# Performance work log

Hardware: AMD Instinct MI355X
Metric: run time of the kernel (lower is better)

Reference implementation:

```python
import jax, jax.numpy as jnp
import numpy as np

B, L, D = 512, 200, 128
N_ITEMS = 50001
T_STEPS = 4
TAU = 2.0
STEP = 1
V_TH = 1.0
SG_ALPHA = 4.0  # spikingjelly default surrogate.Sigmoid alpha


@jax.custom_vjp
def spike(x):
    return (x >= 0.0).astype(x.dtype)

def _spike_fwd(x):
    return spike(x), x

def _spike_bwd(x, g):
    s = jax.nn.sigmoid(SG_ALPHA * x)
    return (g * SG_ALPHA * s * (1.0 - s),)

spike.defvjp(_spike_fwd, _spike_bwd)


def lif_multistep(x):
    """Multi-step LIF (hard reset to 0, detach_reset). x: [T, ...] -> spikes [T, ...]."""
    def step(v, xt):
        v = v + (xt - v) / TAU  # charge (v_reset = 0)
        s = spike(v - V_TH)
        v = v - jax.lax.stop_gradient(s) * v  # hard reset, detached spike
        return v, s
    v0 = jnp.zeros_like(x[0])
    _, spikes = jax.lax.scan(step, v0, x)
    return spikes


def layernorm(x, g, b, eps=1e-5):
    m = x.mean(-1, keepdims=True)
    v = x.var(-1, keepdims=True)
    return (x - m) / jnp.sqrt(v + eps) * g + b


def _build_session_graphs(rng):
    lens = rng.integers(50, L + 1, size=B)
    item_seq = np.zeros((B, L), dtype=np.int64)
    for b in range(B):
        item_seq[b, :lens[b]] = rng.integers(1, N_ITEMS, size=lens[b])
    alias = np.zeros((B, L), dtype=np.int64)
    items = np.zeros((B, L), dtype=np.int64)
    A = np.zeros((B, L, 2 * L), dtype=np.float32)
    for b in range(B):
        u = item_seq[b]
        node = np.unique(u)  # sorted
        items[b, :len(node)] = node
        alias[b] = np.searchsorted(node, u)
        uA = np.zeros((L, L), dtype=np.float32)
        for i in range(L - 1):
            if u[i + 1] == 0:
                break
            r = np.searchsorted(node, u[i])
            c = np.searchsorted(node, u[i + 1])
            uA[r, c] = 1.0
        sin = uA.sum(0); sin[sin == 0] = 1.0
        sout = uA.sum(1); sout[sout == 0] = 1.0
        A[b, :, :L] = (uA / sin).T          # u_A_in.T
        A[b, :, L:] = ((uA.T / sout)).T     # u_A_out.T
    mask = item_seq > 0
    return A, alias, items, mask, lens.astype(np.int64)


def setup_inputs() -> dict:
    rng = np.random.default_rng(0)
    A, alias, items, mask, lens = _build_session_graphs(rng)
    stdv = 1.0 / np.sqrt(D)
    key = jax.random.key(0)
    ks = jax.random.split(key, 24)
    u = lambda k, shape: jax.random.uniform(k, shape, jnp.float32, -stdv, stdv)
    item_emb = u(ks[0], (N_ITEMS, D)).at[0].set(0.0)  # padding_idx=0
    return {
        "A": jnp.asarray(A),
        "alias_inputs": jnp.asarray(alias),
        "items": jnp.asarray(items),
        "mask": jnp.asarray(mask),
        "item_seq_len": jnp.asarray(lens),
        "item_emb": item_emb,
        "W_in": u(ks[1], (D, D)), "b_in": u(ks[2], (D,)),
        "W_out": u(ks[3], (D, D)), "b_out": u(ks[4], (D,)),
        "w_ih": u(ks[5], (3 * D, 2 * D)), "w_hh": u(ks[6], (3 * D, D)),
        "b_ih": u(ks[7], (3 * D,)), "b_hh": u(ks[8], (3 * D,)),
        "b_iah": u(ks[9], (D,)), "b_ioh": u(ks[10], (D,)),
        "W1": u(ks[11], (D, D)), "W2": u(ks[12], (D, D)),
        "W3": u(ks[13], (1, D)), "Wt": u(ks[14], (D, 2 * D)),
        "g_q": u(ks[15], (D,)), "beta_q": u(ks[16], (D,)),
        "g_sh": u(ks[17], (2 * D,)), "beta_sh": u(ks[18], (2 * D,)),
    }


def _forward(A, alias_inputs, items, mask, item_seq_len, item_emb,
             W_in, b_in, W_out, b_out, w_ih, w_hh, b_ih, b_hh, b_iah, b_ioh,
             W1, W2, W3, Wt, g_q, beta_q, g_sh, beta_sh):
    hidden = item_emb[items]  # [B,L,D]
    for _ in range(STEP):
        ein = hidden @ W_in.T + b_in
        eout = hidden @ W_out.T + b_out
        input_in = jnp.einsum('bij,bjd->bid', A[:, :, :L], ein) + b_iah
        input_out = jnp.einsum('bij,bjd->bid', A[:, :, L:], eout) + b_ioh
        inputs = jnp.concatenate([input_in, input_out], axis=-1)  # [B,L,2D]
        gi = inputs @ w_ih.T + b_ih  # [B,L,3D]
        gh = hidden @ w_hh.T + b_hh
        i_r, i_i, i_n = jnp.split(gi, 3, axis=-1)
        h_r, h_i, h_n = jnp.split(gh, 3, axis=-1)
        r = jax.nn.sigmoid(i_r + h_r)
        z = jax.nn.sigmoid(i_i + h_i)
        n = jnp.tanh(i_n + r * h_n)
        hidden = (1.0 - z) * hidden + z * n
    seq_hidden = jnp.take_along_axis(hidden, alias_inputs[..., None], axis=1)  # [B,L,D]
    ht = jnp.take_along_axis(seq_hidden, (item_seq_len - 1)[:, None, None], axis=1)[:, 0]  # [B,D]
    Qb = (ht @ W1.T)[:, None, :] + seq_hidden @ W2.T  # [B,L,D]
    Q = jnp.broadcast_to(Qb[None], (T_STEPS, B, L, D))
    Qs = lif_multistep(layernorm(Q, g_q, beta_q))
    alpha = Qs @ W3.T  # [T,B,L,1]
    mf = mask.astype(alpha.dtype)
    a = jnp.sum(alpha * seq_hidden[None] * mf[None, :, :, None], axis=2)  # [T,B,D]
    ht_T = jnp.broadcast_to(ht[None], (T_STEPS, B, D))
    sh = jnp.concatenate([a, ht_T], axis=-1)  # [T,B,2D]
    sh = layernorm(lif_multistep(sh), g_sh, beta_sh)
    return (sh @ Wt.T).mean(0)  # [B,D]


def reference(A, alias_inputs, items, mask, item_seq_len, item_emb,
              W_in, b_in, W_out, b_out, w_ih, w_hh, b_ih, b_hh, b_iah, b_ioh,
              W1, W2, W3, Wt, g_q, beta_q, g_sh, beta_sh):
    return _forward(A, alias_inputs, items, mask, item_seq_len, item_emb,
                    W_in, b_in, W_out, b_out, w_ih, w_hh, b_ih, b_hh, b_iah, b_ioh,
                    W1, W2, W3, Wt, g_q, beta_q, g_sh, beta_sh)
```

## Files before the change

kernel.cpp:

```cpp
#include <hip/hip_runtime.h>
#include <hip/hip_bf16.h>
#include <cstdint>
#include <cstddef>

#define B_ 512
#define L_ 200
#define D_ 128
#define M_ (B_*L_)
#define T_ 4

typedef short bf16x8 __attribute__((ext_vector_type(8)));
typedef unsigned short u16x8 __attribute__((ext_vector_type(8)));
typedef float f32x4 __attribute__((ext_vector_type(4)));

__device__ __forceinline__ float bf2f(unsigned short u){
  union { unsigned int i; float f; } c; c.i = ((unsigned int)u)<<16; return c.f;
}
__device__ __forceinline__ unsigned short f2bf(float f){
  union { float f; unsigned int i; } c; c.f = f;
  unsigned int r = c.i + 0x7FFFu + ((c.i>>16)&1u);
  return (unsigned short)(r>>16);
}
__device__ __forceinline__ float wsum(float v){
  #pragma unroll
  for (int m=1;m<64;m<<=1) v += __shfl_xor(v, m, 64);
  return v;
}
__device__ __forceinline__ void gload_lds16(const void* g, void* l){
  __builtin_amdgcn_global_load_lds(
      (const __attribute__((address_space(1))) void*)g,
      (__attribute__((address_space(3))) void*)l, 16, 0, 0);
}

__global__ __launch_bounds__(128)
void k_prepW(const float* __restrict__ w_ih, const float* __restrict__ w_hh,
             const float* __restrict__ W_in, const float* __restrict__ W_out,
             const float* __restrict__ b_in, const float* __restrict__ b_out,
             const float* __restrict__ b_ih, const float* __restrict__ b_hh,
             const float* __restrict__ b_iah, const float* __restrict__ b_ioh,
             const float* __restrict__ W2,
             const int* __restrict__ alias, const int* __restrict__ lens,
             unsigned short* __restrict__ Wbig, float* __restrict__ biasBase,
             float* __restrict__ uIn, float* __restrict__ uOut,
             unsigned short* __restrict__ w2b, int* __restrict__ nb)
{
  const int p = blockIdx.x, t = threadIdx.x;
  if (p < 128) w2b[p*128 + t] = f2bf(W2[p*128 + t]);
  const int dim = p>>2, g = p&3;
  const int row = (g==0) ? dim : (g==1) ? 128+dim : 256+dim;
  const bool has_ih = (g!=3), has_hh = (g!=2);
  __shared__ float wl[128], wrg[128], red[3][128];
  wl[t]  = has_ih ? w_ih[(size_t)row*256 + t]       : 0.f;
  wrg[t] = has_ih ? w_ih[(size_t)row*256 + 128 + t] : 0.f;
  __syncthreads();
  float cin = 0.f, cout = 0.f;
  if (has_ih) {
    for (int m=0;m<128;m++){
      cin  += wl[m]  * W_in [m*128 + t];
      cout += wrg[m] * W_out[m*128 + t];
    }
  }
  Wbig[(size_t)p*384 +       t] = f2bf(cin);
  Wbig[(size_t)p*384 + 128 + t] = f2bf(cout);
  Wbig[(size_t)p*384 + 256 + t] = f2bf(has_hh ? w_hh[(size_t)row*128 + t] : 0.f);
  red[0][t] = wl[t]*b_iah[t] + wrg[t]*b_ioh[t];
  red[1][t] = wl[t]*b_in[t];
  red[2][t] = wrg[t]*b_out[t];
  __syncthreads();
  if (t == 0) {
    float v=0.f, ui=0.f, uo=0.f;
    for (int k=0;k<128;k++){ v += red[0][k]; ui += red[1][k]; uo += red[2][k]; }
    float bb;
    if (g==0)      bb = b_ih[dim]     + b_hh[dim]     + v;
    else if (g==1) bb = b_ih[128+dim] + b_hh[128+dim] + v;
    else if (g==2) bb = b_ih[256+dim] + v;
    else           bb = b_hh[256+dim];
    biasBase[p] = bb;
    uIn[p]  = has_ih ? ui : 0.f;
    uOut[p] = has_ih ? uo : 0.f;
  }
  if (t < 64) {
    const int len = lens[p];
    int m = 0;
    for (int l=t; l<len; l+=64) m = max(m, alias[p*L_ + l]);
    #pragma unroll
    for (int o=1;o<64;o<<=1) m = max(m, __shfl_xor(m, o, 64));
    if (t==0) nb[p] = m + 1;
  }
}

__global__ __launch_bounds__(512)
void k_scan(const int* __restrict__ nb, const int* __restrict__ lens,
            int* __restrict__ nbase, int* __restrict__ vbase)
{
  __shared__ int A[2][512], Bv[2][512];
  const int t = threadIdx.x;
  const int a0 = nb[t], b0 = lens[t];
  A[0][t] = a0; Bv[0][t] = b0;
  __syncthreads();
  int cur = 0;
  for (int off=1; off<512; off<<=1){
    const int nxt = cur^1;
    A[nxt][t]  = A[cur][t]  + (t>=off ? A[cur][t-off]  : 0);
    Bv[nxt][t] = Bv[cur][t] + (t>=off ? Bv[cur][t-off] : 0);
    __syncthreads();
    cur = nxt;
  }
  nbase[t] = A[cur][t] - a0;
  vbase[t] = Bv[cur][t] - b0;
  if (t==511){ nbase[512] = A[cur][511]; vbase[512] = Bv[cur][511]; }
}

__global__ __launch_bounds__(1024)
void k_aggemb(const int* __restrict__ alias, const int* __restrict__ items,
              const int* __restrict__ lens, const float* __restrict__ emb,
              const int* __restrict__ nb, const int* __restrict__ nbase,
              const int* __restrict__ vbase,
              unsigned short* __restrict__ X3, unsigned char* __restrict__ cf,
              int* __restrict__ gidx)
{
  const int b = blockIdx.x, tid = threadIdx.x;
  __shared__ unsigned short hl[L_*128];
  __shared__ int al[L_], it[L_];
  __shared__ unsigned bmIn[L_*8], bmOut[L_*8];
  if (tid < L_) { al[tid] = alias[b*L_ + tid]; it[tid] = items[b*L_ + tid]; }
  for (int i=tid; i<L_*8; i+=1024){ bmIn[i]=0u; bmOut[i]=0u; }
  __syncthreads();
  const int len = lens[b], nB = nb[b], base = nbase[b];
  if (tid < len) gidx[vbase[b] + tid] = base + al[tid];
  if (tid < len-1) {
    const int r = al[tid], c = al[tid+1];
    atomicOr(&bmIn[c*8 + (r>>5)],  1u<<(r&31));
    atomicOr(&bmOut[r*8 + (c>>5)], 1u<<(c&31));
  }
  const int rr = tid>>5, cc = (tid&31)<<2;
  for (int s=0; s<nB; s+=32) {
    const int j = s + rr;
    if (j < nB) {
      const float4 v = *(const float4*)(emb + (size_t)it[j]*128 + cc);
      ushort4 o; o.x=f2bf(v.x); o.y=f2bf(v.y); o.z=f2bf(v.z); o.w=f2bf(v.w);
      *(ushort4*)(hl + j*128 + cc) = o;
      *(ushort4*)(X3 + (size_t)(base + j)*384 + 256 + cc) = o;
    }
  }
  __syncthreads();
  const int g = tid >> 7, d = tid & 127;
  for (int s=0; s<nB; s+=8) {
    const int i = s + g;
    if (i < nB) {
      float si=0.f, so=0.f; int ci=0, co=0;
      #pragma unroll
      for (int wd=0; wd<8; ++wd) {
        unsigned word = bmIn[i*8+wd];
        while (word) { int j = __ffs(word)-1; word &= word-1u;
          si += bf2f(hl[(wd*32+j)*128 + d]); ci++; }
        word = bmOut[i*8+wd];
        while (word) { int j = __ffs(word)-1; word &= word-1u;
          so += bf2f(hl[(wd*32+j)*128 + d]); co++; }
      }
      unsigned short* xr = X3 + (size_t)(base + i)*384;
      xr[d]       = f2bf(si / (float)(ci>0?ci:1));
      xr[128 + d] = f2bf(so / (float)(co>0?co:1));
      if (d == 0) cf[base + i] = (unsigned char)((ci>0?1:0) | (co>0?2:0));
    }
  }
}

__global__ __launch_bounds__(512)
void k_gates_q0(const unsigned short* __restrict__ X3,
                const unsigned short* __restrict__ Wbig,
                const unsigned short* __restrict__ w2b,
                const float* __restrict__ biasBase,
                const float* __restrict__ uIn,
                const float* __restrict__ uOut,
                const unsigned char* __restrict__ cf,
                unsigned short* __restrict__ hidden,
                unsigned short* __restrict__ q0n,
                const int* __restrict__ mlimit)
{
  const int m0 = blockIdx.x * 128;
  if (m0 >= *mlimit) return;
  __shared__ __align__(16) short sA[2][128*32];
  __shared__ __align__(16) short sB[2][512*32];
  const int tid = threadIdx.x;
  const int lane = tid & 63;
  const int w = tid >> 6;
  const int wr  = (w>>2)*64;
  const int wcp = (w&3)*128;
  const int fr = lane & 15;
  const int fq = lane >> 4;
  const int fk = ((fq ^ ((fr>>1)&3))&3)<<3;

  f32x4 acc[4][8];
  #pragma unroll
  for (int i=0;i<4;i++)
    #pragma unroll
    for (int j=0;j<8;j++) acc[i][j] = (f32x4){0.f,0.f,0.f,0.f};

  const int rA = tid>>2, sAx = tid&3;
  const int kA = ((sAx ^ ((rA>>1)&3))&3)<<3;

  auto stage = [&](int t){
    const int buf = t & 1, ks = t << 5;
    gload_lds16(X3 + (size_t)(m0 + rA)*384 + ks + kA, sA[buf] + (size_t)tid*8);
    #pragma unroll
    for (int q=0;q<4;q++){
      const int cB = tid + q*512;
      const int rB = cB>>2, sBx = cB&3;
      const int kB = ((sBx ^ ((rB>>1)&3))&3)<<3;
      gload_lds16(Wbig + (size_t)rB*384 + ks + kB, sB[buf] + (size_t)cB*8);
    }
  };
  stage(0);
  __syncthreads();
  for (int t=0; t<12; ++t){
    if (t < 11) stage(t+1);
    const short* a_ = sA[t&1];
    const short* b_ = sB[t&1];
    bf16x8 af[4], bfr[8];
    #pragma unroll
    for (int i=0;i<4;i++)
      af[i]  = *(const bf16x8*)(a_ + (wr  + i*16 + fr)*32 + fk);
    #pragma unroll
    for (int j=0;j<8;j++)
      bfr[j] = *(const bf16x8*)(b_ + (wcp + j*16 + fr)*32 + fk);
    #pragma unroll
    for (int i=0;i<4;i++)
      #pragma unroll
      for (int j=0;j<8;j++)
        acc[i][j] = __builtin_amdgcn_mfma_f32_16x16x32_bf16(af[i], bfr[j], acc[i][j], 0,0,0);
    __syncthreads();
  }

  short* hl  = sB[0];
  short* w2l = sB[1];

  #pragma unroll
  for (int q=0;q<4;q++){
    const int cW = tid + q*512;
    const int rW = cW>>4, sW = cW&15;
    gload_lds16(w2b + (size_t)rW*128 + ((sW ^ (rW&7))<<3), w2l + (size_t)cW*8);
  }

  const bool q0b = (lane & 1), q1b = (lane & 2);
  #pragma unroll
  for (int j=0;j<8;j++){
    const int dim = (w&3)*32 + j*4 + ((lane>>2)&3);
    const float4 bb = *(const float4*)(biasBase + dim*4);
    const float4 bi = *(const float4*)(uIn  + dim*4);
    const float4 bo = *(const float4*)(uOut + dim*4);
    #pragma unroll
    for (int i=0;i<4;i++){
      const float a0=acc[i][j][0], a1=acc[i][j][1], a2=acc[i][j][2], a3=acc[i][j][3];
      const float t0=__shfl_xor(a0,1), t1=__shfl_xor(a1,1), t2=__shfl_xor(a2,1), t3=__shfl_xor(a3,1);
      const float s0 = q0b? t1:a0, s1 = q0b? a1:t0, s2 = q0b? t3:a2, s3 = q0b? a3:t2;
      const float u0=__shfl_xor(s0,2), u1=__shfl_xor(s1,2), u2=__shfl_xor(s2,2), u3=__shfl_xor(s3,2);
      float G0 = q1b? u2:s0, G1 = q1b? u3:s1, G2 = q1b? s2:u0, G3 = q1b? s3:u1;
      const int row = m0 + wr + i*16 + fq*4 + (lane&3);
      const unsigned c = cf[row];
      const float fi = (c&1) ? 1.f : 0.f, fo = (c&2) ? 1.f : 0.f;
      G0 += bb.x + fi*bi.x + fo*bo.x;
      G1 += bb.y + fi*bi.y + fo*bo.y;
      G2 += bb.z + fi*bi.z + fo*bo.z;
      G3 += bb.w;
      const float h = bf2f(X3[(size_t)row*384 + 256 + dim]);
      const float r = 1.f/(1.f+__expf(-G0));
      const float z = 1.f/(1.f+__expf(-G1));
      const float x = G2 + r*G3;
      const float n = 1.f - 2.f/(__expf(2.f*x)+1.f);
      const unsigned short hv = f2bf((1.f-z)*h + z*n);
      hidden[(size_t)row*128 + dim] = hv;
      const int rl = row - m0;
      hl[rl*128 + (((dim>>3) ^ (rl&7))<<3) + (dim&7)] = hv;
    }
  }
  __syncthreads();

  f32x4 acc2[4][2];
  #pragma unroll
  for (int i=0;i<4;i++){ acc2[i][0]=(f32x4){0,0,0,0}; acc2[i][1]=(f32x4){0,0,0,0}; }
  const int wc2 = (w&3)*32;
  #pragma unroll
  for (int kk=0;kk<4;kk++){
    bf16x8 af2[4], bf2_[2];
    #pragma unroll
    for (int i=0;i<4;i++){
      const int r = wr + i*16 + fr;
      af2[i] = *(const bf16x8*)(hl + r*128 + (((kk*4 + fq) ^ (r&7))<<3));
    }
    #pragma unroll
    for (int j=0;j<2;j++){
      const int c = wc2 + j*16 + fr;
      bf2_[j] = *(const bf16x8*)(w2l + c*128 + (((kk*4 + fq) ^ (c&7))<<3));
    }
    #pragma unroll
    for (int i=0;i<4;i++)
      #pragma unroll
      for (int j=0;j<2;j++)
        acc2[i][j] = __builtin_amdgcn_mfma_f32_16x16x32_bf16(af2[i], bf2_[j], acc2[i][j], 0,0,0);
  }
  #pragma unroll
  for (int i=0;i<4;i++){
    #pragma unroll
    for (int j=0;j<2;j++){
      const int col = wc2 + j*16 + fr;
      #pragma unroll
      for (int v=0;v<4;v++){
        const int row = m0 + wr + i*16 + fq*4 + v;
        q0n[(size_t)row*128 + col] = f2bf(acc2[i][j][v]);
      }
    }
  }
}

__global__ __launch_bounds__(1024)
void k_attn(const unsigned short* __restrict__ q0n,
            const unsigned short* __restrict__ hidden, const int* __restrict__ gidx,
            const int* __restrict__ lens, const int* __restrict__ vbase,
            const float* __restrict__ W1,
            const float* __restrict__ g_q, const float* __restrict__ beta_q,
            const float* __restrict__ W3,
            const float* __restrict__ g_sh, const float* __restrict__ beta_sh,
            const float* __restrict__ Wt, float* __restrict__ out)
{
  const int b = blockIdx.x, tid = threadIdx.x;
  const int w = tid>>6, lane = tid&63;
  __shared__ float a_acc[16][T_][128];
  __shared__ float htv[128], htw[128];
  __shared__ float ys[256];
  __shared__ float part[T_][4];
  const int len = lens[b], vb = vbase[b];
  for (int i=tid; i<16*T_*128; i+=1024) ((float*)a_acc)[i] = 0.f;
  if (tid < 128) htv[tid] = bf2f(hidden[(size_t)gidx[vb + len - 1]*128 + tid]);
  __syncthreads();
  {
    const int d = tid >> 3, seg = (tid & 7) << 4;
    const float* wr1 = W1 + (size_t)d*128 + seg;
    const float* hv = htv + seg;
    float p = 0.f;
    #pragma unroll
    for (int k=0;k<16;k++) p += wr1[k]*hv[k];
    p += __shfl_xor(p, 1, 64); p += __shfl_xor(p, 2, 64); p += __shfl_xor(p, 4, 64);
    if ((tid & 7) == 0) htw[d] = p;
  }
  __syncthreads();
  const float h0 = htw[lane], h1 = htw[lane+64];
  const float gq0 = g_q[lane], gq1 = g_q[lane+64];
  const float bq0 = beta_q[lane], bq1 = beta_q[lane+64];
  const float w30 = W3[lane], w31 = W3[lane+64];
  for (int l = w; l < len; l += 16) {
    const size_t row = (size_t)(vb + l);
    const size_t hrow = (size_t)gidx[row];
    const float q0 = bf2f(q0n[hrow*128 + lane]) + h0;
    const float q1 = bf2f(q0n[hrow*128 + lane + 64]) + h1;
    const float m = wsum(q0+q1) * (1.f/128.f);
    const float d0 = q0-m, d1 = q1-m;
    const float var = wsum(d0*d0 + d1*d1) * (1.f/128.f);
    const float inv = rsqrtf(var + 1e-5f);
    const float x0 = d0*inv*gq0 + bq0;
    const float x1 = d1*inv*gq1 + bq1;
    const float sh0 = bf2f(hidden[hrow*128+lane]), sh1 = bf2f(hidden[hrow*128+lane+64]);
    float v0=0.f, v1=0.f;
    #pragma unroll
    for (int t=0;t<T_;t++){
      v0 = 0.5f*(v0+x0); v1 = 0.5f*(v1+x1);
      const float s0 = (v0>=1.f)?1.f:0.f, s1 = (v1>=1.f)?1.f:0.f;
      v0 -= s0*v0; v1 -= s1*v1;
      const float alpha = wsum(s0*w30 + s1*w31);
      a_acc[w][t][lane] += alpha*sh0; a_acc[w][t][lane+64] += alpha*sh1;
    }
  }
  __syncthreads();

  float sp[T_] = {0.f,0.f,0.f,0.f};
  if (tid < 256) {
    const float xh = (tid >= 128) ? htv[tid-128] : 0.f;
    float v = 0.f;
    #pragma unroll
    for (int t=0;t<T_;t++){
      float x;
      if (tid < 128) {
        x = 0.f;
        #pragma unroll
        for (int p=0;p<16;p++) x += a_acc[p][t][tid];
      } else x = xh;
      v = 0.5f*(v + x);
      const float s = (v>=1.f)?1.f:0.f;
      v -= s*v;
      sp[t] = s;
    }
    #pragma unroll
    for (int t=0;t<T_;t++){
      const float r = wsum(sp[t]);
      if (lane==0) part[t][w] = r;
    }
  }
  __syncthreads();
  if (tid < 256) {
    float acc4 = 0.f;
    #pragma unroll
    for (int t=0;t<T_;t++){
      const float k = part[t][0]+part[t][1]+part[t][2]+part[t][3];
      const float mean = k * (1.f/256.f);
      const float varr = mean - mean*mean;
      const float inv = rsqrtf(varr + 1e-5f);
      acc4 += (sp[t]-mean)*inv;
    }
    ys[tid] = acc4*g_sh[tid] + 4.f*beta_sh[tid];
  }
  __syncthreads();
  if (tid < 128) {
    float acc = 0.f;
    const float4* wr4 = (const float4*)(Wt + (size_t)tid*256);
    const float4* ys4 = (const float4*)ys;
    #pragma unroll 8
    for (int k=0;k<64;k++){
      const float4 wv = wr4[k], yv = ys4[k];
      acc += wv.x*yv.x + wv.y*yv.y + wv.z*yv.z + wv.w*yv.w;
    }
    out[(size_t)b*128 + tid] = acc*0.25f;
  }
}

extern "C" void kernel_launch(void* const* d_in, const int* in_sizes, int n_in,
                              void* d_out, int out_size, void* d_ws, size_t ws_size,
                              hipStream_t stream)
{
  const int*   alias  = (const int*)d_in[1];
  const int*   items  = (const int*)d_in[2];
  const int*   lens   = (const int*)d_in[4];
  const float* emb    = (const float*)d_in[5];
  const float* W_in   = (const float*)d_in[6];
  const float* b_in   = (const float*)d_in[7];
  const float* W_out  = (const float*)d_in[8];
  const float* b_out  = (const float*)d_in[9];
  const float* w_ih   = (const float*)d_in[10];
  const float* w_hh   = (const float*)d_in[11];
  const float* b_ih   = (const float*)d_in[12];
  const float* b_hh   = (const float*)d_in[13];
  const float* b_iah  = (const float*)d_in[14];
  const float* b_ioh  = (const float*)d_in[15];
  const float* W1     = (const float*)d_in[16];
  const float* W2     = (const float*)d_in[17];
  const float* W3     = (const float*)d_in[18];
  const float* Wt     = (const float*)d_in[19];
  const float* g_q    = (const float*)d_in[20];
  const float* beta_q = (const float*)d_in[21];
  const float* g_sh   = (const float*)d_in[22];
  const float* beta_sh= (const float*)d_in[23];

  char* ws = (char*)d_ws;
  size_t off = 0;
  auto alloc = [&](size_t bytes)->void* {
    void* p = ws + off; off += (bytes + 255) & ~(size_t)255; return p;
  };
  unsigned short* X3    = (unsigned short*)alloc((size_t)M_*384*2);
  unsigned short* hidden= (unsigned short*)alloc((size_t)M_*128*2);
  unsigned short* q0n   = (unsigned short*)alloc((size_t)M_*128*2);
  int*            gidx  = (int*)alloc((size_t)M_*4);
  unsigned short* Wbig  = (unsigned short*)alloc((size_t)512*384*2);
  unsigned short* w2b   = (unsigned short*)alloc(16384*2);
  float*          biasBase = (float*)alloc(512*4);
  float*          uIn   = (float*)alloc(512*4);
  float*          uOut  = (float*)alloc(512*4);
  unsigned char*  cf    = (unsigned char*)alloc(M_);
  int*            nb    = (int*)alloc(512*4);
  int*            nbase = (int*)alloc(513*4);
  int*            vbase = (int*)alloc(513*4);
  if (off > ws_size) return;

  k_prepW<<<512,128,0,stream>>>(w_ih,w_hh,W_in,W_out,b_in,b_out,b_ih,b_hh,
                                b_iah,b_ioh,W2,alias,lens,
                                Wbig,biasBase,uIn,uOut,w2b,nb);
  k_scan<<<1,512,0,stream>>>(nb, lens, nbase, vbase);
  k_aggemb<<<B_,1024,0,stream>>>(alias, items, lens, emb, nb, nbase, vbase,
                                 X3, cf, gidx);
  k_gates_q0<<<800,512,0,stream>>>(X3, Wbig, w2b, biasBase, uIn, uOut, cf,
                                   hidden, q0n, nbase+512);
  k_attn<<<B_,1024,0,stream>>>(q0n, hidden, gidx, lens, vbase, W1, g_q, beta_q,
                               W3, g_sh, beta_sh, Wt, (float*)d_out);
}
```

Baseline: 203.2 us.

## Split gates GEMM into two column halves to cut LDS and registers

The fused GRU-gates kernel now computes its 512-wide gate GEMM in two passes of 256 columns. This halves the B-tile shared memory and the accumulator registers per pass, which can raise occupancy. First-half hidden values are packed into registers until the shared buffer is free, and the W2 operand is read straight from global memory into registers instead of being staged in LDS. The cost is reloading and recomputing the A tile (X3) twice, plus extra synchronisation between the passes.

Result: no change. 203.7 us (+0.2%).

```diff
diff --git a/kernel.cpp b/kernel.cpp
--- a/kernel.cpp
+++ b/kernel.cpp
@@ -181,123 +181,133 @@
   const int m0 = blockIdx.x * 128;
   if (m0 >= *mlimit) return;
   __shared__ __align__(16) short sA[2][128*32];
-  __shared__ __align__(16) short sB[2][512*32];
+  __shared__ __align__(16) short sB[2][256*32];
   const int tid = threadIdx.x;
   const int lane = tid & 63;
   const int w = tid >> 6;
   const int wr  = (w>>2)*64;
-  const int wcp = (w&3)*128;
+  const int wcp = (w&3)*64;
   const int fr = lane & 15;
   const int fq = lane >> 4;
   const int fk = ((fq ^ ((fr>>1)&3))&3)<<3;
 
-  f32x4 acc[4][8];
-  #pragma unroll
-  for (int i=0;i<4;i++)
-    #pragma unroll
-    for (int j=0;j<8;j++) acc[i][j] = (f32x4){0.f,0.f,0.f,0.f};
-
-  const int rA = tid>>2, sAx = tid&3;
-  const int kA = ((sAx ^ ((rA>>1)&3))&3)<<3;
-
-  auto stage = [&](int t){
-    const int buf = t & 1, ks = t << 5;
-    gload_lds16(X3 + (size_t)(m0 + rA)*384 + ks + kA, sA[buf] + (size_t)tid*8);
-    #pragma unroll
-    for (int q=0;q<4;q++){
-      const int cB = tid + q*512;
-      const int rB = cB>>2, sBx = cB&3;
-      const int kB = ((sBx ^ ((rB>>1)&3))&3)<<3;
-      gload_lds16(Wbig + (size_t)rB*384 + ks + kB, sB[buf] + (size_t)cB*8);
-    }
-  };
-  stage(0);
-  __syncthreads();
-  for (int t=0; t<12; ++t){
-    if (t < 11) stage(t+1);
-    const short* a_ = sA[t&1];
-    const short* b_ = sB[t&1];
-    bf16x8 af[4], bfr[8];
+  const int ra = tid>>2, sa_ = tid&3, ka = ((sa_ ^ ((ra>>1)&3))&3)<<3;
+  const int c1 = tid + 512, rb1 = c1>>2, sb1 = c1&3, kb1 = ((sb1 ^ ((rb1>>1)&3))&3)<<3;
+
+  short* hl = &sB[0][0];
+  unsigned hv0p[8];
+  const bool q0b_ = (lane & 1), q1b_ = (lane & 2);
+
+  for (int half=0; half<2; ++half){
+    const int p0 = half << 8;
+    f32x4 acc[4][4];
     #pragma unroll
     for (int i=0;i<4;i++)
-      af[i]  = *(const bf16x8*)(a_ + (wr  + i*16 + fr)*32 + fk);
-    #pragma unroll
-    for (int j=0;j<8;j++)
-      bfr[j] = *(const bf16x8*)(b_ + (wcp + j*16 + fr)*32 + fk);
-    #pragma unroll
-    for (int i=0;i<4;i++)
-      #pragma unroll
-      for (int j=0;j<8;j++)
-        acc[i][j] = __builtin_amdgcn_mfma_f32_16x16x32_bf16(af[i], bfr[j], acc[i][j], 0,0,0);
+      #pragma unroll
+      for (int j=0;j<4;j++) acc[i][j] = (f32x4){0.f,0.f,0.f,0.f};
+
+    auto stage = [&](int t){
+      const int buf = t & 1, ks = t << 5;
+      gload_lds16(X3   + (size_t)(m0 + ra )*384 + ks + ka , sA[buf] + (size_t)tid*8);
+      gload_lds16(Wbig + (size_t)(p0 + ra )*384 + ks + ka , sB[buf] + (size_t)tid*8);
+      gload_lds16(Wbig + (size_t)(p0 + rb1)*384 + ks + kb1, sB[buf] + 4096 + (size_t)tid*8);
+    };
+    stage(0);
     __syncthreads();
-  }
-
-  short* hl  = sB[0];
-  short* w2l = sB[1];
-
-  #pragma unroll
-  for (int q=0;q<4;q++){
-    const int cW = tid + q*512;
-    const int rW = cW>>4, sW = cW&15;
-    gload_lds16(w2b + (size_t)rW*128 + ((sW ^ (rW&7))<<3), w2l + (size_t)cW*8);
-  }
-
-  const bool q0b = (lane & 1), q1b = (lane & 2);
-  #pragma unroll
-  for (int j=0;j<8;j++){
-    const int dim = (w&3)*32 + j*4 + ((lane>>2)&3);
-    const float4 bb = *(const float4*)(biasBase + dim*4);
-    const float4 bi = *(const float4*)(uIn  + dim*4);
-    const float4 bo = *(const float4*)(uOut + dim*4);
+    for (int t=0; t<12; ++t){
+      if (t < 11) stage(t+1);
+      const short* a_ = sA[t&1];
+      const short* b_ = sB[t&1];
+      bf16x8 af[4], bfr[4];
+      #pragma unroll
+      for (int i=0;i<4;i++){
+        af[i]  = *(const bf16x8*)(a_ + (wr  + i*16 + fr)*32 + fk);
+        bfr[i] = *(const bf16x8*)(b_ + (wcp + i*16 + fr)*32 + fk);
+      }
+      #pragma unroll
+      for (int i=0;i<4;i++)
+        #pragma unroll
+        for (int j=0;j<4;j++)
+          acc[i][j] = __builtin_amdgcn_mfma_f32_16x16x32_bf16(af[i], bfr[j], acc[i][j], 0,0,0);
+      __syncthreads();
+    }
+
+    #pragma unroll
+    for (int j=0;j<4;j++){
+      const int dim = half*64 + (w&3)*16 + j*4 + ((lane>>2)&3);
+      const float4 bb = *(const float4*)(biasBase + dim*4);
+      const float4 bi = *(const float4*)(uIn  + dim*4);
+      const float4 bo = *(const float4*)(uOut + dim*4);
+      #pragma unroll
+      for (int i=0;i<4;i++){
+        const float a0=acc[i][j][0], a1=acc[i][j][1], a2=acc[i][j][2], a3=acc[i][j][3];
+        const float t0=__shfl_xor(a0,1), t1=__shfl_xor(a1,1), t2=__shfl_xor(a2,1), t3=__shfl_xor(a3,1);
+        const float s0 = q0b_? t1:a0, s1 = q0b_? a1:t0, s2 = q0b_? t3:a2, s3 = q0b_? a3:t2;
+        const float u0=__shfl_xor(s0,2), u1=__shfl_xor(s1,2), u2=__shfl_xor(s2,2), u3=__shfl_xor(s3,2);
+        float G0 = q1b_? u2:s0, G1 = q1b_? u3:s1, G2 = q1b_? s2:u0, G3 = q1b_? s3:u1;
+        const int row = m0 + wr + i*16 + fq*4 + (lane&3);
+        const unsigned c = cf[row];
+        const float fi = (c&1) ? 1.f : 0.f, fo = (c&2) ? 1.f : 0.f;
+        G0 += bb.x + fi*bi.x + fo*bo.x;
+        G1 += bb.y + fi*bi.y + fo*bo.y;
+        G2 += bb.z + fi*bi.z + fo*bo.z;
+        G3 += bb.w;
+        const float h = bf2f(X3[(size_t)row*384 + 256 + dim]);
+        const float r = 1.f/(1.f+__expf(-G0));
+        const float z = 1.f/(1.f+__expf(-G1));
+        const float x = G2 + r*G3;
+        const float n = 1.f - 2.f/(__expf(2.f*x)+1.f);
+        const unsigned short hvv = f2bf((1.f-z)*h + z*n);
+        hidden[(size_t)row*128 + dim] = hvv;
+        if (half == 0) {
+          const int pi = j*2 + (i>>1);
+          if ((i&1)==0) hv0p[pi] = hvv;
+          else          hv0p[pi] |= ((unsigned)hvv << 16);
+        } else {
+          const int rl = row - m0;
+          hl[rl*128 + (((dim>>3) ^ (rl&7))<<3) + (dim&7)] = (short)hvv;
+        }
+      }
+    }
+  }
+
+  #pragma unroll
+  for (int j=0;j<4;j++){
+    const int dim = (w&3)*16 + j*4 + ((lane>>2)&3);
     #pragma unroll
     for (int i=0;i<4;i++){
-      const float a0=acc[i][j][0], a1=acc[i][j][1], a2=acc[i][j][2], a3=acc[i][j][3];
-      const float t0=__shfl_xor(a0,1), t1=__shfl_xor(a1,1), t2=__shfl_xor(a2,1), t3=__shfl_xor(a3,1);
-      const float s0 = q0b? t1:a0, s1 = q0b? a1:t0, s2 = q0b? t3:a2, s3 = q0b? a3:t2;
-      const float u0=__shfl_xor(s0,2), u1=__shfl_xor(s1,2), u2=__shfl_xor(s2,2), u3=__shfl_xor(s3,2);
-      float G0 = q1b? u2:s0, G1 = q1b? u3:s1, G2 = q1b? s2:u0, G3 = q1b? s3:u1;
-      const int row = m0 + wr + i*16 + fq*4 + (lane&3);
-      const unsigned c = cf[row];
-      const float fi = (c&1) ? 1.f : 0.f, fo = (c&2) ? 1.f : 0.f;
-      G0 += bb.x + fi*bi.x + fo*bo.x;
-      G1 += bb.y + fi*bi.y + fo*bo.y;
-      G2 += bb.z + fi*bi.z + fo*bo.z;
-      G3 += bb.w;
-      const float h = bf2f(X3[(size_t)row*384 + 256 + dim]);
-      const float r = 1.f/(1.f+__expf(-G0));
-      const float z = 1.f/(1.f+__expf(-G1));
-      const float x = G2 + r*G3;
-      const float n = 1.f - 2.f/(__expf(2.f*x)+1.f);
-      const unsigned short hv = f2bf((1.f-z)*h + z*n);
-      hidden[(size_t)row*128 + dim] = hv;
-      const int rl = row - m0;
-      hl[rl*128 + (((dim>>3) ^ (rl&7))<<3) + (dim&7)] = hv;
-    }
-  }
+      const int rl = wr + i*16 + fq*4 + (lane&3);
+      const unsigned short hvv =
+        (unsigned short)((i&1) ? (hv0p[j*2+(i>>1)] >> 16) : (hv0p[j*2+(i>>1)] & 0xFFFFu));
+      hl[rl*128 + (((dim>>3) ^ (rl&7))<<3) + (dim&7)] = (short)hvv;
+    }
+  }
+
+  const int wc2 = (w&3)*32;
+  bf16x8 bw[2][4];
+  #pragma unroll
+  for (int j=0;j<2;j++)
+    #pragma unroll
+    for (int kk=0;kk<4;kk++)
+      bw[j][kk] = *(const bf16x8*)(w2b + (size_t)(wc2 + j*16 + fr)*128 + kk*32 + fq*8);
   __syncthreads();
 
   f32x4 acc2[4][2];
   #pragma unroll
   for (int i=0;i<4;i++){ acc2[i][0]=(f32x4){0,0,0,0}; acc2[i][1]=(f32x4){0,0,0,0}; }
-  const int wc2 = (w&3)*32;
   #pragma unroll
   for (int kk=0;kk<4;kk++){
-    bf16x8 af2[4], bf2_[2];
+    bf16x8 af2[4];
     #pragma unroll
     for (int i=0;i<4;i++){
       const int r = wr + i*16 + fr;
       af2[i] = *(const bf16x8*)(hl + r*128 + (((kk*4 + fq) ^ (r&7))<<3));
     }
     #pragma unroll
-    for (int j=0;j<2;j++){
-      const int c = wc2 + j*16 + fr;
-      bf2_[j] = *(const bf16x8*)(w2l + c*128 + (((kk*4 + fq) ^ (c&7))<<3));
-    }
-    #pragma unroll
     for (int i=0;i<4;i++)
       #pragma unroll
       for (int j=0;j<2;j++)
-        acc2[i][j] = __builtin_amdgcn_mfma_f32_16x16x32_bf16(af2[i], bf2_[j], acc2[i][j], 0,0,0);
+        acc2[i][j] = __builtin_amdgcn_mfma_f32_16x16x32_bf16(af2[i], bw[j][kk], acc2[i][j], 0,0,0);
   }
   #pragma unroll
   for (int i=0;i<4;i++){
```
